# Performance work log

Hardware: AMD Instinct MI355X
Metric: run time of the kernel (lower is better)

The kernel has to match this reference:

```python
import jax, jax.numpy as jnp
import numpy as np

N_HOPS = 2
LEAKY_SLOPE = 0.2
EPS = 1e-12


def setup_inputs() -> dict:
    key = jax.random.key(0)
    k1, k2, k3, k4, k5, k6 = jax.random.split(key, 6)
    N, R, C, E = 100000, 50, 64, 1000000
    return {
        "entity_emb": jax.random.normal(k1, (N, C), dtype=jnp.float32) * 0.1,
        "relation_emb": jax.random.normal(k2, (R, C), dtype=jnp.float32) * 0.1,
        "fc_w": jax.random.normal(k3, (C, 2 * C), dtype=jnp.float32) * 0.1,  # torch Linear weight [out, in]
        "fc_b": jax.random.normal(k4, (C,), dtype=jnp.float32) * 0.1,
        "edge_index": jax.random.randint(k5, (2, E), 0, N, dtype=jnp.int64),
        "edge_type": jax.random.randint(k6, (E,), 0, R, dtype=jnp.int64),
    }


def reference(entity_emb, relation_emb, fc_w, fc_b, edge_index, edge_type):
    """RGAT.forward with mess_dropout=False: n_hops of relational-attention
    gather -> leakyrelu -> scatter_softmax(head) -> scatter_sum -> residual -> L2 normalize."""
    N = entity_emb.shape[0]
    head, tail = edge_index[0], edge_index[1]
    rel_e = relation_emb[edge_type]  # [E, C]

    def agg(emb):
        a_input = jnp.concatenate([emb[head], emb[tail]], axis=-1)  # [E, 2C]
        h = a_input @ fc_w.T + fc_b                                  # fc(a_input): [E, C]
        e = jnp.sum(h * rel_e, axis=-1)                              # [E]
        e = jnp.where(e > 0, e, LEAKY_SLOPE * e)                     # leakyrelu(0.2)
        # scatter_softmax over head segments (numerically stable)
        m = jax.ops.segment_max(e, head, num_segments=N)             # [N]
        ex = jnp.exp(e - m[head])
        denom = jax.ops.segment_sum(ex, head, num_segments=N)        # [N]
        w = ex / denom[head]                                         # [E]
        agg_emb = jax.ops.segment_sum(emb[tail] * w[:, None], head, num_segments=N)
        agg_emb = agg_emb + emb                                      # residual
        return agg_emb

    emb = entity_emb
    for _ in range(N_HOPS):
        emb = agg(emb)
        # F.normalize(emb): L2 along dim=1 with eps clamp
        nrm = jnp.sqrt(jnp.sum(emb * emb, axis=-1, keepdims=True))
        emb = emb / jnp.maximum(nrm, EPS)
    return emb
```

## Files before the change

### kernel.cpp

```cpp
#include <hip/hip_runtime.h>

#define C 64
#define RMAX 50
#define LEAKY 0.2f
#define CAP 48

__device__ __forceinline__ float bf2f(unsigned short u) {
  return __uint_as_float(((unsigned)u) << 16);
}
__device__ __forceinline__ unsigned short f2bf(float x) {
  unsigned u = __float_as_uint(x);
  return (unsigned short)((u + 0x7FFFu + ((u >> 16) & 1u)) >> 16);
}

__device__ __forceinline__ int wave_isbf(const void* ent) {
  const unsigned* w = (const unsigned*)ent;
  const int lane = threadIdx.x & 63;
  int ok = 0;
#pragma unroll
  for (int i = 0; i < 4; ++i) {
    unsigned lo = w[lane + 64 * i] & 0xFFFFu;
    float a = fabsf(__uint_as_float(lo << 16));
    ok += (lo == 0u || (a >= 1e-9f && a <= 1e9f)) ? 1 : 0;
  }
#pragma unroll
  for (int d = 1; d < 64; d <<= 1) ok += __shfl_xor(ok, d, 64);
  return ok >= 224;
}
__device__ __forceinline__ int wave_is64(const int* p) {
  const int lane = threadIdx.x & 63;
  int z = (p[2 * lane + 1] == 0) ? 1 : 0;
#pragma unroll
  for (int d = 1; d < 64; d <<= 1) z += __shfl_xor(z, d, 64);
  return z >= 62;
}
__device__ __forceinline__ float loadF(const void* p, int i, int isbf) {
  return isbf ? bf2f(((const unsigned short*)p)[i]) : ((const float*)p)[i];
}

__global__ void uvc_kernel(const void* __restrict__ rel,
                           const void* __restrict__ fcw,
                           const void* __restrict__ fcb,
                           float* __restrict__ U, float* __restrict__ V,
                           float* __restrict__ cvec) {
  const int isbf = wave_isbf(rel);
  const int r = blockIdx.x;
  const int i = threadIdx.x;
  float acc = 0.f;
  for (int o = 0; o < C; ++o)
    acc += loadF(rel, r * C + o, isbf) * loadF(fcw, o * (2 * C) + i, isbf);
  if (i < C) U[r * C + i] = acc;
  else       V[r * C + (i - C)] = acc;
  if (i < C) {
    float p = loadF(rel, r * C + i, isbf) * loadF(fcb, i, isbf);
#pragma unroll
    for (int d = 1; d < 64; d <<= 1) p += __shfl_xor(p, d, 64);
    if (i == 0) cvec[r] = p;
  }
}

__global__ void conv_kernel(const void* __restrict__ ent, unsigned* __restrict__ dst,
                            int n8) {
  const int isbf = wave_isbf(ent);
  int i = blockIdx.x * blockDim.x + threadIdx.x;
  if (i >= n8) return;
  uint4 o;
  if (isbf) {
    o = ((const uint4*)ent)[i];
  } else {
    const float4* q = (const float4*)ent;
    float4 a = q[2 * i], b = q[2 * i + 1];
    o.x = (unsigned)f2bf(a.x) | ((unsigned)f2bf(a.y) << 16);
    o.y = (unsigned)f2bf(a.z) | ((unsigned)f2bf(a.w) << 16);
    o.z = (unsigned)f2bf(b.x) | ((unsigned)f2bf(b.y) << 16);
    o.w = (unsigned)f2bf(b.z) | ((unsigned)f2bf(b.w) << 16);
  }
  ((uint4*)dst)[i] = o;
}

__global__ void fillb_kernel(const int* __restrict__ eidx, const int* __restrict__ etype,
                             int* __restrict__ cnt, int* __restrict__ packed,
                             int E, int N, int Rc) {
  const int is64 = wave_is64(eidx);
  const int et64 = wave_is64(etype);
  const int base = (blockIdx.x * blockDim.x + threadIdx.x) * 4;
  int h[4], t[4], r[4];
#pragma unroll
  for (int k = 0; k < 4; ++k) {
    const int e = base + k;
    if (e < E) {
      h[k] = is64 ? eidx[2 * e] : eidx[e];
      t[k] = is64 ? eidx[2 * E + 2 * e] : eidx[E + e];
      r[k] = et64 ? etype[2 * e] : etype[e];
    }
  }
  int pos[4];
#pragma unroll
  for (int k = 0; k < 4; ++k) {
    const int e = base + k;
    if (e < E) {
      if ((unsigned)h[k] >= (unsigned)N) h[k] = 0;
      pos[k] = atomicAdd(&cnt[h[k]], 1);
    }
  }
#pragma unroll
  for (int k = 0; k < 4; ++k) {
    const int e = base + k;
    if (e < E && pos[k] < CAP) {
      int tt = t[k]; if ((unsigned)tt >= (unsigned)N) tt = 0;
      int rr = r[k]; if ((unsigned)rr >= (unsigned)Rc) rr = 0;
      packed[h[k] * CAP + pos[k]] = tt | (rr << 20);
    }
  }
}

__global__ void fillA_kernel(const int* __restrict__ eidx, const int* __restrict__ etype,
                             int* __restrict__ bcnt, int2* __restrict__ bbuf,
                             int E, int N, int Rc, int shift, int nbuck, int bcap) {
  __shared__ int lh[256];
  __shared__ int gbase[256];
  const int is64 = wave_is64(eidx);
  const int et64 = wave_is64(etype);
  const int tid = threadIdx.x;
  if (tid < 256) lh[tid] = 0;
  const int eBase = blockIdx.x * 2048;
  int h[8], tr[8], bk[8], lp[8], ok[8];
  __syncthreads();
#pragma unroll
  for (int k = 0; k < 8; ++k) {
    const int e = eBase + k * 256 + tid;
    ok[k] = (e < E);
    if (ok[k]) {
      int hh = is64 ? eidx[2 * e] : eidx[e];
      int tt = is64 ? eidx[2 * E + 2 * e] : eidx[E + e];
      int rr = et64 ? etype[2 * e] : etype[e];
      if ((unsigned)hh >= (unsigned)N) hh = 0;
      if ((unsigned)tt >= (unsigned)N) tt = 0;
      if ((unsigned)rr >= (unsigned)Rc) rr = 0;
      h[k] = hh; tr[k] = tt | (rr << 20);
      bk[k] = hh >> shift;
      lp[k] = atomicAdd(&lh[bk[k]], 1);
    }
  }
  __syncthreads();
  if (tid < nbuck) gbase[tid] = lh[tid] ? atomicAdd(&bcnt[tid], lh[tid]) : 0;
  __syncthreads();
#pragma unroll
  for (int k = 0; k < 8; ++k) {
    if (ok[k]) {
      int posb = gbase[bk[k]] + lp[k];
      if (posb < bcap) bbuf[(size_t)bk[k] * bcap + posb] = make_int2(h[k], tr[k]);
    }
  }
}

__global__ void fillB_kernel(const int* __restrict__ bcnt, const int2* __restrict__ bbuf,
                             int* __restrict__ cnt, int* __restrict__ packed,
                             int N, int bcap) {
  const int b = blockIdx.x;
  int bc = bcnt[b]; if (bc > bcap) bc = bcap;
  const int2* src = &bbuf[(size_t)b * bcap];
  for (int k = threadIdx.x; k < bc; k += blockDim.x) {
    int2 e = src[k];
    int h = e.x; if ((unsigned)h >= (unsigned)N) h = 0;
    int pos = atomicAdd(&cnt[h], 1);
    if (pos < CAP) packed[h * CAP + pos] = e.y;
  }
}

__global__ void histo_kernel(const int* __restrict__ cnt, int* __restrict__ hist, int N) {
  __shared__ int histS[65];
  const int tid = threadIdx.x;
  for (int k = tid; k < 65; k += 1024) histS[k] = 0;
  __syncthreads();
  const int i = blockIdx.x * 1024 + tid;
  if (i < N) {
    int b = cnt[i]; if (b > 64) b = 64;
    atomicAdd(&histS[b], 1);
  }
  __syncthreads();
  for (int k = tid; k < 65; k += 1024)
    if (histS[k]) atomicAdd(&hist[k], histS[k]);
}

__global__ void order_kernel(const int* __restrict__ cnt, const int* __restrict__ hist,
                             int* __restrict__ bincur, int* __restrict__ order, int N) {
  __shared__ int binstart[66];
  __shared__ int lh[65];
  __shared__ int lbase[65];
  const int tid = threadIdx.x;
  for (int k = tid; k < 65; k += 1024) { binstart[k] = hist[k]; lh[k] = 0; }
  __syncthreads();
  if (tid == 0) {
    int run = 0;
    for (int k = 0; k < 65; ++k) { int t = binstart[k]; binstart[k] = run; run += t; }
    binstart[65] = run;
  }
  __syncthreads();
  const int i = blockIdx.x * 1024 + tid;
  int b = 0, lpos = 0;
  if (i < N) {
    b = cnt[i]; if (b > 64) b = 64;
    lpos = atomicAdd(&lh[b], 1);
  }
  __syncthreads();
  if (tid < 65) lbase[tid] = lh[tid] ? atomicAdd(&bincur[tid], lh[tid]) : 0;
  __syncthreads();
  if (i < N) {
    int dst = binstart[b] + lbase[b] + lpos;
    if ((unsigned)dst < (unsigned)N) order[dst] = i;
  }
}

__device__ __forceinline__ void unpack8(uint4 u, float4& a, float4& b) {
  a.x = __uint_as_float(u.x << 16); a.y = __uint_as_float(u.x & 0xFFFF0000u);
  a.z = __uint_as_float(u.y << 16); a.w = __uint_as_float(u.y & 0xFFFF0000u);
  b.x = __uint_as_float(u.z << 16); b.y = __uint_as_float(u.z & 0xFFFF0000u);
  b.z = __uint_as_float(u.w << 16); b.w = __uint_as_float(u.w & 0xFFFF0000u);
}

template <bool IN_EXT, bool OUT_EXT>
__global__ __launch_bounds__(256) void hop_kernel(
    const void* __restrict__ emb_in_v, void* __restrict__ emb_out_v,
    const int* __restrict__ cnt, const int* __restrict__ packed,
    const float* __restrict__ Ug, const float* __restrict__ Vg,
    const float* __restrict__ cg, const int* __restrict__ order,
    const void* __restrict__ ent_det, int N, int Rc) {
  int isbf = 1;
  if (IN_EXT || OUT_EXT) isbf = wave_isbf(ent_det);
  const int l = threadIdx.x & 7;
  const int slot = blockIdx.x * 32 + (threadIdx.x >> 3);
  if (slot >= N) return;
  const int n = order[slot];

  auto loadRow = [&](int row, float4& a, float4& b) {
    if (IN_EXT && !isbf) {
      const float4* q = (const float4*)((const float*)emb_in_v + (size_t)row * C);
      a = q[2 * l]; b = q[2 * l + 1];
    } else {
      uint4 u = ((const uint4*)emb_in_v)[(size_t)row * 8 + l];
      unpack8(u, a, b);
    }
  };

  const int start = n * CAP;
  int deg = cnt[n];
  if (deg > CAP) deg = CAP;
  if (deg < 0) deg = 0;

  float4 enA, enB;
  loadRow(n, enA, enB);

  float sum = 0.f;
  float4 accA = {0.f, 0.f, 0.f, 0.f}, accB = {0.f, 0.f, 0.f, 0.f};

  float4 etA, etB, uuA, uuB, vvA, vvB;
  float cb = 0.f;
  auto issue = [&](unsigned pkv) {
    int t = (int)(pkv & 0xFFFFFu); if (t >= N) t = 0;
    int r = (int)(pkv >> 20);      if (r >= Rc) r = 0;
    loadRow(t, etA, etB);
    const float4* uq = (const float4*)&Ug[r * C + l * 8];
    const float4* vq = (const float4*)&Vg[r * C + l * 8];
    uuA = uq[0]; uuB = uq[1];
    vvA = vq[0]; vvB = vq[1];
    cb = cg[r];
  };
  if (deg > 0) issue((unsigned)packed[start]);
  int pknext = (deg > 1) ? packed[start + 1] : 0;

  for (int jj = 0; jj < deg; ++jj) {
    const float4 cetA = etA, cetB = etB;
    const float4 cuuA = uuA, cuuB = uuB, cvvA = vvA, cvvB = vvB;
    const float ccb = cb;
    if (jj + 1 < deg) issue((unsigned)pknext);
    if (jj + 2 < deg) pknext = packed[start + jj + 2];

    float p = cuuA.x * enA.x + cuuA.y * enA.y + cuuA.z * enA.z + cuuA.w * enA.w
            + cuuB.x * enB.x + cuuB.y * enB.y + cuuB.z * enB.z + cuuB.w * enB.w
            + cvvA.x * cetA.x + cvvA.y * cetA.y + cvvA.z * cetA.z + cvvA.w * cetA.w
            + cvvB.x * cetB.x + cvvB.y * cetB.y + cvvB.z * cetB.z + cvvB.w * cetB.w;
    p += __shfl_xor(p, 1); p += __shfl_xor(p, 2); p += __shfl_xor(p, 4);
    float s = p + ccb;
    s = s > 0.f ? s : LEAKY * s;
    const float wgt = __expf(fminf(s, 50.f));
    sum += wgt;
    accA.x += wgt * cetA.x; accA.y += wgt * cetA.y;
    accA.z += wgt * cetA.z; accA.w += wgt * cetA.w;
    accB.x += wgt * cetB.x; accB.y += wgt * cetB.y;
    accB.z += wgt * cetB.z; accB.w += wgt * cetB.w;
  }

  const float inv = (deg > 0) ? 1.0f / sum : 0.f;
  float4 oA, oB;
  oA.x = accA.x * inv + enA.x; oA.y = accA.y * inv + enA.y;
  oA.z = accA.z * inv + enA.z; oA.w = accA.w * inv + enA.w;
  oB.x = accB.x * inv + enB.x; oB.y = accB.y * inv + enB.y;
  oB.z = accB.z * inv + enB.z; oB.w = accB.w * inv + enB.w;

  float ss = oA.x * oA.x + oA.y * oA.y + oA.z * oA.z + oA.w * oA.w
           + oB.x * oB.x + oB.y * oB.y + oB.z * oB.z + oB.w * oB.w;
  ss += __shfl_xor(ss, 1); ss += __shfl_xor(ss, 2); ss += __shfl_xor(ss, 4);
  const float sc = 1.0f / fmaxf(sqrtf(ss), 1e-12f);
  oA.x *= sc; oA.y *= sc; oA.z *= sc; oA.w *= sc;
  oB.x *= sc; oB.y *= sc; oB.z *= sc; oB.w *= sc;

  if (OUT_EXT && !isbf) {
    float4* q = (float4*)((float*)emb_out_v + (size_t)n * C);
    q[2 * l] = oA; q[2 * l + 1] = oB;
  } else {
    uint4 u;
    u.x = (unsigned)f2bf(oA.x) | ((unsigned)f2bf(oA.y) << 16);
    u.y = (unsigned)f2bf(oA.z) | ((unsigned)f2bf(oA.w) << 16);
    u.z = (unsigned)f2bf(oB.x) | ((unsigned)f2bf(oB.y) << 16);
    u.w = (unsigned)f2bf(oB.z) | ((unsigned)f2bf(oB.w) << 16);
    ((uint4*)emb_out_v)[(size_t)n * 8 + l] = u;
  }
}

extern "C" void kernel_launch(void* const* d_in, const int* in_sizes, int n_in,
                              void* d_out, int out_size, void* d_ws, size_t ws_size,
                              hipStream_t stream) {
  const void* ent  = d_in[0];
  const void* rel  = d_in[1];
  const void* fcw  = d_in[2];
  const void* fcb  = d_in[3];
  const int* eidx  = (const int*)d_in[4];
  const int* etype = (const int*)d_in[5];

  const int N  = in_sizes[0] / C;
  const int R0 = in_sizes[1] / C;
  const int Rc = R0 < RMAX ? R0 : RMAX;
  const int E  = in_sizes[5];
  const int nbN = (N + 1023) / 1024;
  (void)n_in; (void)out_size;

  int shift = 9;
  while ((((N - 1) >> shift) + 1) > 256) shift++;
  const int nbuck = ((N - 1) >> shift) + 1;
  int bcap = (E + nbuck - 1) / nbuck;
  bcap += bcap / 4 + 256;

  char* ws = (char*)d_ws;
  size_t off = 0;
  auto alloc = [&](size_t bytes) -> void* {
    void* p = ws + off;
    off = (off + bytes + 255) & ~(size_t)255;
    return p;
  };
  int*   cnt    = (int*)alloc(((size_t)N + 512) * 4);
  int*   hist   = cnt + N;
  int*   bincur = hist + 128;
  int*   bcnt   = bincur + 128;
  float* U      = (float*)alloc((size_t)Rc * C * 4);
  float* V      = (float*)alloc((size_t)Rc * C * 4);
  float* cv     = (float*)alloc((size_t)Rc * 4);
  int*   order  = (int*)alloc((size_t)N * 4);
  int*   packed = (int*)alloc((size_t)N * CAP * 4);
  const size_t emb0B   = (size_t)N * C * 2;
  const size_t bucketB = (size_t)nbuck * bcap * 8;
  const size_t midB    = (size_t)N * C * 2;
  const size_t base    = off;
  const size_t align = 256;
  const bool tier2 = base + ((emb0B > bucketB ? emb0B : bucketB) + align) + (midB + align) <= ws_size;
  const bool tier1 = base + (emb0B + align) + (midB + align) <= ws_size;

  void* unionbuf = alloc(tier2 ? (emb0B > bucketB ? emb0B : bucketB)
                                : (tier1 ? emb0B : 0));
  unsigned short* mid = (unsigned short*)alloc(midB);
  unsigned short* emb0 = (unsigned short*)unionbuf;
  int2* bbuf = (int2*)unionbuf;

  hipMemsetAsync(cnt, 0, ((size_t)N + 512) * 4, stream);
  uvc_kernel<<<Rc, 128, 0, stream>>>(rel, fcw, fcb, U, V, cv);

  if (tier2) {
    fillA_kernel<<<(E + 2047) / 2048, 256, 0, stream>>>(eidx, etype, bcnt, bbuf,
                                                        E, N, Rc, shift, nbuck, bcap);
    fillB_kernel<<<nbuck, 256, 0, stream>>>(bcnt, bbuf, cnt, packed, N, bcap);
  } else {
    fillb_kernel<<<(E + 1023) / 1024, 256, 0, stream>>>(eidx, etype, cnt, packed, E, N, Rc);
  }
  histo_kernel<<<nbN, 1024, 0, stream>>>(cnt, hist, N);
  order_kernel<<<nbN, 1024, 0, stream>>>(cnt, hist, bincur, order, N);

  const int hb = (N + 31) / 32;
  if (tier1 || tier2) {
    const int n8 = N * C / 8;
    conv_kernel<<<(n8 + 255) / 256, 256, 0, stream>>>(ent, (unsigned*)emb0, n8);
    hop_kernel<false, false><<<hb, 256, 0, stream>>>(emb0, mid, cnt, packed, U, V, cv, order, ent, N, Rc);
  } else {
    hop_kernel<true,  false><<<hb, 256, 0, stream>>>(ent, mid, cnt, packed, U, V, cv, order, ent, N, Rc);
  }
  hop_kernel<false, true ><<<hb, 256, 0, stream>>>(mid, d_out, cnt, packed, U, V, cv, order, ent, N, Rc);
}
```

Before: 242.0 us.

## Batch hop edge loads by four, pad global counters, split bucket fill across blocks

The hop kernel now reads four packed edges at once with an int4 load and issues all four neighbour-row gathers before computing, which replaces the one-ahead software prefetch and raises memory-level parallelism. The global counters (bucket, histogram, bin cursors) are spaced 16 ints apart so contended atomics fall on separate cache lines. fillA handles 1024 edges per block instead of 2048, and fillB uses four blocks per bucket. The degree order is reversed so high-degree nodes are scheduled first. Risks: more registers per thread in the hop kernel, and int4 reads that can run past deg into unused slots, which are masked by zero weights.

```diff
diff --git a/kernel.cpp b/kernel.cpp
--- a/kernel.cpp
+++ b/kernel.cpp
@@ -123,11 +123,11 @@
   const int et64 = wave_is64(etype);
   const int tid = threadIdx.x;
   if (tid < 256) lh[tid] = 0;
-  const int eBase = blockIdx.x * 2048;
-  int h[8], tr[8], bk[8], lp[8], ok[8];
-  __syncthreads();
-#pragma unroll
-  for (int k = 0; k < 8; ++k) {
+  const int eBase = blockIdx.x * 1024;
+  int h[4], tr[4], bk[4], lp[4], ok[4];
+  __syncthreads();
+#pragma unroll
+  for (int k = 0; k < 4; ++k) {
     const int e = eBase + k * 256 + tid;
     ok[k] = (e < E);
     if (ok[k]) {
@@ -143,10 +143,10 @@
     }
   }
   __syncthreads();
-  if (tid < nbuck) gbase[tid] = lh[tid] ? atomicAdd(&bcnt[tid], lh[tid]) : 0;
-  __syncthreads();
-#pragma unroll
-  for (int k = 0; k < 8; ++k) {
+  if (tid < nbuck) gbase[tid] = lh[tid] ? atomicAdd(&bcnt[tid * 16], lh[tid]) : 0;
+  __syncthreads();
+#pragma unroll
+  for (int k = 0; k < 4; ++k) {
     if (ok[k]) {
       int posb = gbase[bk[k]] + lp[k];
       if (posb < bcap) bbuf[(size_t)bk[k] * bcap + posb] = make_int2(h[k], tr[k]);
@@ -157,10 +157,11 @@
 __global__ void fillB_kernel(const int* __restrict__ bcnt, const int2* __restrict__ bbuf,
                              int* __restrict__ cnt, int* __restrict__ packed,
                              int N, int bcap) {
-  const int b = blockIdx.x;
-  int bc = bcnt[b]; if (bc > bcap) bc = bcap;
+  const int b = blockIdx.x >> 2;
+  const int sub = blockIdx.x & 3;
+  int bc = bcnt[b * 16]; if (bc > bcap) bc = bcap;
   const int2* src = &bbuf[(size_t)b * bcap];
-  for (int k = threadIdx.x; k < bc; k += blockDim.x) {
+  for (int k = sub * 256 + threadIdx.x; k < bc; k += 1024) {
     int2 e = src[k];
     int h = e.x; if ((unsigned)h >= (unsigned)N) h = 0;
     int pos = atomicAdd(&cnt[h], 1);
@@ -180,7 +181,7 @@
   }
   __syncthreads();
   for (int k = tid; k < 65; k += 1024)
-    if (histS[k]) atomicAdd(&hist[k], histS[k]);
+    if (histS[k]) atomicAdd(&hist[k * 16], histS[k]);
 }
 
 __global__ void order_kernel(const int* __restrict__ cnt, const int* __restrict__ hist,
@@ -189,11 +190,11 @@
   __shared__ int lh[65];
   __shared__ int lbase[65];
   const int tid = threadIdx.x;
-  for (int k = tid; k < 65; k += 1024) { binstart[k] = hist[k]; lh[k] = 0; }
+  for (int k = tid; k < 65; k += 1024) { binstart[k] = hist[k * 16]; lh[k] = 0; }
   __syncthreads();
   if (tid == 0) {
     int run = 0;
-    for (int k = 0; k < 65; ++k) { int t = binstart[k]; binstart[k] = run; run += t; }
+    for (int k = 64; k >= 0; --k) { int t = binstart[k]; binstart[k] = run; run += t; }
     binstart[65] = run;
   }
   __syncthreads();
@@ -204,7 +205,7 @@
     lpos = atomicAdd(&lh[b], 1);
   }
   __syncthreads();
-  if (tid < 65) lbase[tid] = lh[tid] ? atomicAdd(&bincur[tid], lh[tid]) : 0;
+  if (tid < 65) lbase[tid] = lh[tid] ? atomicAdd(&bincur[tid * 16], lh[tid]) : 0;
   __syncthreads();
   if (i < N) {
     int dst = binstart[b] + lbase[b] + lpos;
@@ -254,41 +255,50 @@
   float sum = 0.f;
   float4 accA = {0.f, 0.f, 0.f, 0.f}, accB = {0.f, 0.f, 0.f, 0.f};
 
-  float4 etA, etB, uuA, uuB, vvA, vvB;
-  float cb = 0.f;
-  auto issue = [&](unsigned pkv) {
-    int t = (int)(pkv & 0xFFFFFu); if (t >= N) t = 0;
-    int r = (int)(pkv >> 20);      if (r >= Rc) r = 0;
-    loadRow(t, etA, etB);
-    const float4* uq = (const float4*)&Ug[r * C + l * 8];
-    const float4* vq = (const float4*)&Vg[r * C + l * 8];
-    uuA = uq[0]; uuB = uq[1];
-    vvA = vq[0]; vvB = vq[1];
-    cb = cg[r];
-  };
-  if (deg > 0) issue((unsigned)packed[start]);
-  int pknext = (deg > 1) ? packed[start + 1] : 0;
-
-  for (int jj = 0; jj < deg; ++jj) {
-    const float4 cetA = etA, cetB = etB;
-    const float4 cuuA = uuA, cuuB = uuB, cvvA = vvA, cvvB = vvB;
-    const float ccb = cb;
-    if (jj + 1 < deg) issue((unsigned)pknext);
-    if (jj + 2 < deg) pknext = packed[start + jj + 2];
-
-    float p = cuuA.x * enA.x + cuuA.y * enA.y + cuuA.z * enA.z + cuuA.w * enA.w
-            + cuuB.x * enB.x + cuuB.y * enB.y + cuuB.z * enB.z + cuuB.w * enB.w
-            + cvvA.x * cetA.x + cvvA.y * cetA.y + cvvA.z * cetA.z + cvvA.w * cetA.w
-            + cvvB.x * cetB.x + cvvB.y * cetB.y + cvvB.z * cetB.z + cvvB.w * cetB.w;
-    p += __shfl_xor(p, 1); p += __shfl_xor(p, 2); p += __shfl_xor(p, 4);
-    float s = p + ccb;
-    s = s > 0.f ? s : LEAKY * s;
-    const float wgt = __expf(fminf(s, 50.f));
-    sum += wgt;
-    accA.x += wgt * cetA.x; accA.y += wgt * cetA.y;
-    accA.z += wgt * cetA.z; accA.w += wgt * cetA.w;
-    accB.x += wgt * cetB.x; accB.y += wgt * cetB.y;
-    accB.z += wgt * cetB.z; accB.w += wgt * cetB.w;
+  int4 pk = (deg > 0) ? *(const int4*)&packed[start] : make_int4(0, 0, 0, 0);
+  for (int j0 = 0; j0 < deg; j0 += 4) {
+    const int4 cur = pk;
+    if (j0 + 4 < deg) pk = *(const int4*)&packed[start + j0 + 4];
+
+    int tt[4], rr[4];
+    tt[0] = cur.x & 0xFFFFF; rr[0] = (int)((unsigned)cur.x >> 20);
+    tt[1] = cur.y & 0xFFFFF; rr[1] = (int)((unsigned)cur.y >> 20);
+    tt[2] = cur.z & 0xFFFFF; rr[2] = (int)((unsigned)cur.z >> 20);
+    tt[3] = cur.w & 0xFFFFF; rr[3] = (int)((unsigned)cur.w >> 20);
+#pragma unroll
+    for (int k = 0; k < 4; ++k) {
+      if (tt[k] >= N) tt[k] = 0;
+      if (rr[k] >= Rc) rr[k] = 0;
+    }
+    float4 eA[4], eB[4];
+#pragma unroll
+    for (int k = 0; k < 4; ++k) loadRow(tt[k], eA[k], eB[k]);
+    float4 uA[4], uB[4], vA[4], vB[4];
+    float cbv[4];
+#pragma unroll
+    for (int k = 0; k < 4; ++k) {
+      const float4* uq = (const float4*)&Ug[rr[k] * C + l * 8];
+      const float4* vq = (const float4*)&Vg[rr[k] * C + l * 8];
+      uA[k] = uq[0]; uB[k] = uq[1];
+      vA[k] = vq[0]; vB[k] = vq[1];
+      cbv[k] = cg[rr[k]];
+    }
+#pragma unroll
+    for (int k = 0; k < 4; ++k) {
+      float p = uA[k].x * enA.x + uA[k].y * enA.y + uA[k].z * enA.z + uA[k].w * enA.w
+              + uB[k].x * enB.x + uB[k].y * enB.y + uB[k].z * enB.z + uB[k].w * enB.w
+              + vA[k].x * eA[k].x + vA[k].y * eA[k].y + vA[k].z * eA[k].z + vA[k].w * eA[k].w
+              + vB[k].x * eB[k].x + vB[k].y * eB[k].y + vB[k].z * eB[k].z + vB[k].w * eB[k].w;
+      p += __shfl_xor(p, 1); p += __shfl_xor(p, 2); p += __shfl_xor(p, 4);
+      float s = p + cbv[k];
+      s = s > 0.f ? s : LEAKY * s;
+      const float wgt = (j0 + k < deg) ? __expf(fminf(s, 50.f)) : 0.f;
+      sum += wgt;
+      accA.x += wgt * eA[k].x; accA.y += wgt * eA[k].y;
+      accA.z += wgt * eA[k].z; accA.w += wgt * eA[k].w;
+      accB.x += wgt * eB[k].x; accB.y += wgt * eB[k].y;
+      accB.z += wgt * eB[k].z; accB.w += wgt * eB[k].w;
+    }
   }
 
   const float inv = (deg > 0) ? 1.0f / sum : 0.f;
@@ -348,10 +358,10 @@
     off = (off + bytes + 255) & ~(size_t)255;
     return p;
   };
-  int*   cnt    = (int*)alloc(((size_t)N + 512) * 4);
+  int*   cnt    = (int*)alloc(((size_t)N + 1040 + 1040 + 4096 + 64) * 4);
   int*   hist   = cnt + N;
-  int*   bincur = hist + 128;
-  int*   bcnt   = bincur + 128;
+  int*   bincur = hist + 1040;
+  int*   bcnt   = bincur + 1040;
   float* U      = (float*)alloc((size_t)Rc * C * 4);
   float* V      = (float*)alloc((size_t)Rc * C * 4);
   float* cv     = (float*)alloc((size_t)Rc * 4);
@@ -371,13 +381,13 @@
   unsigned short* emb0 = (unsigned short*)unionbuf;
   int2* bbuf = (int2*)unionbuf;
 
-  hipMemsetAsync(cnt, 0, ((size_t)N + 512) * 4, stream);
+  hipMemsetAsync(cnt, 0, ((size_t)N + 1040 + 1040 + 4096 + 64) * 4, stream);
   uvc_kernel<<<Rc, 128, 0, stream>>>(rel, fcw, fcb, U, V, cv);
 
   if (tier2) {
-    fillA_kernel<<<(E + 2047) / 2048, 256, 0, stream>>>(eidx, etype, bcnt, bbuf,
+    fillA_kernel<<<(E + 1023) / 1024, 256, 0, stream>>>(eidx, etype, bcnt, bbuf,
                                                         E, N, Rc, shift, nbuck, bcap);
-    fillB_kernel<<<nbuck, 256, 0, stream>>>(bcnt, bbuf, cnt, packed, N, bcap);
+    fillB_kernel<<<nbuck * 4, 256, 0, stream>>>(bcnt, bbuf, cnt, packed, N, bcap);
   } else {
     fillb_kernel<<<(E + 1023) / 1024, 256, 0, stream>>>(eidx, etype, cnt, packed, E, N, Rc);
   }
```

Result: no change. 243.3 us (+0.5%).
